# Kernel tuning notes

Measured on AMD Instinct MI355X. Metric: run time of the kernel, lower is better.

The kernel has to match this reference:

```python
import jax, jax.numpy as jnp
import numpy as np

TOKENS = 16384
HID = 2048


def _per_channel_scale(w, b):
    # scale per output channel, as in _apply_per_channel_scaling
    s = jnp.clip(jnp.max(jnp.abs(w), axis=1), 1e-6, None)  # [out]
    return w / s[:, None], b / s, s[None, :]  # scaled weight, scaled bias, scale row-vector


def setup_inputs() -> dict:
    key = jax.random.key(0)
    k = jax.random.split(key, 5)
    x = jax.random.normal(k[0], (TOKENS, HID), dtype=jnp.float32)
    w1_raw = jax.random.normal(k[1], (2 * HID, HID), dtype=jnp.float32) * 0.02
    b1_raw = jax.random.normal(k[2], (2 * HID,), dtype=jnp.float32) * 0.02
    w2_raw = jax.random.normal(k[3], (HID, 2 * HID), dtype=jnp.float32) * 0.02
    b2_raw = jax.random.normal(k[4], (HID,), dtype=jnp.float32) * 0.02
    w1, b1, s1 = _per_channel_scale(w1_raw, b1_raw)
    w2, b2, s2 = _per_channel_scale(w2_raw, b2_raw)
    return {"x": x, "w1": w1, "b1": b1, "s1": s1, "w2": w2, "b2": b2, "s2": s2}


def reference(x, w1, b1, s1, w2, b2, s2):
    # fc1 (scaled weights) -> per-channel dequant scale -> exact GELU -> fc2 -> scale
    h = (x @ w1.T + b1) * s1            # [T, 2H]
    h = jax.nn.gelu(h, approximate=False)
    y = (h @ w2.T + b2) * s2            # [T, H]
    return y
```

## Files before the change

### kernel.cpp

```cpp
#include <hip/hip_runtime.h>
#include <math.h>

typedef __attribute__((ext_vector_type(8))) short short8;
typedef __attribute__((ext_vector_type(4))) float f32x4;

#define GLOBAL_AS __attribute__((address_space(1)))
#define LDS_AS __attribute__((address_space(3)))

__device__ __forceinline__ unsigned short f2bf(float f) {
  union { float f; unsigned u; } v; v.f = f;
  unsigned r = v.u + 0x7fffu + ((v.u >> 16) & 1u);
  return (unsigned short)(r >> 16);
}

__global__ void cvt_f32_to_bf16(const float* __restrict__ in,
                                unsigned short* __restrict__ out, int n4) {
  int i = blockIdx.x * blockDim.x + threadIdx.x;
  if (i < n4) {
    const float4 v = ((const float4*)in)[i];
    ushort4 o;
    o.x = f2bf(v.x); o.y = f2bf(v.y); o.z = f2bf(v.z); o.w = f2bf(v.w);
    ((ushort4*)out)[i] = o;
  }
}

template <int EPI>
__global__ __launch_bounds__(512, 2) void gemm256_8ph(
    const unsigned short* __restrict__ A, const unsigned short* __restrict__ B,
    const float* __restrict__ bias, const float* __restrict__ scale,
    void* __restrict__ Cout, int M, int N, int K) {
  constexpr int BM = 256, BN = 256;
  __shared__ __attribute__((aligned(16))) unsigned short ldsA[4][8192];
  __shared__ __attribute__((aligned(16))) unsigned short ldsB[4][8192];

  const int NT = K >> 6;
  const int nTn = N / BN;
  const int bid = blockIdx.x;
  const int cpx = gridDim.x >> 3;
  const int wg = (bid & 7) * cpx + (bid >> 3);
  const int tm = wg / nTn, tn = wg % nTn;

  const int tid = threadIdx.x;
  const int w = tid >> 6, l = tid & 63;
  const int wr = w >> 2, wc = w & 3;
  const int lr = l & 15, g = l >> 4;

  const unsigned short* Ag = A + (size_t)tm * BM * K;
  const unsigned short* Bg = B + (size_t)tn * BN * K;

  size_t gs[2];
#pragma unroll
  for (int sgi = 0; sgi < 2; ++sgi) {
    int p = tid * 16 + sgi * 8192;
    int sp = p ^ (((p >> 7) & 7) << 4);
    gs[sgi] = (size_t)(sp >> 6) * K + ((sp & 63) >> 1);
  }
  const int ldsWaveOff = w * 512;

  auto STAGE = [&](int tau, int ks, const unsigned short* gb,
                   unsigned short (*slotArr)[8192]) {
    if (tau >= NT) return;
    unsigned short* sl = slotArr[(2 * tau + ks) & 3];
    const size_t ko = ((size_t)tau << 6) + (ks << 5);
    __builtin_amdgcn_global_load_lds((const GLOBAL_AS void*)(gb + gs[0] + ko),
                                     (LDS_AS void*)(sl + ldsWaveOff), 16, 0, 0);
    __builtin_amdgcn_global_load_lds((const GLOBAL_AS void*)(gb + gs[1] + ko),
                                     (LDS_AS void*)(sl + 4096 + ldsWaveOff), 16, 0, 0);
  };

  auto LD = [&](const unsigned short* slot, int row) -> short8 {
    int by = row * 64 + g * 16;
    by ^= ((by >> 7) & 7) << 4;
    return *(const short8*)((const char*)slot + by);
  };

  f32x4 acc[8][4] = {};

  STAGE(0, 0, Ag, ldsA); STAGE(0, 0, Bg, ldsB);
  STAGE(0, 1, Ag, ldsA); STAGE(0, 1, Bg, ldsB);
  STAGE(1, 0, Ag, ldsA); STAGE(1, 0, Bg, ldsB);
  asm volatile("s_waitcnt vmcnt(4)" ::: "memory");
  __builtin_amdgcn_s_barrier();

  for (int kt = 0; kt < NT; ++kt) {
    const unsigned short* As0 = ldsA[(2 * kt) & 3];
    const unsigned short* Bs0 = ldsB[(2 * kt) & 3];
    const unsigned short* As1 = ldsA[(2 * kt + 1) & 3];
    const unsigned short* Bs1 = ldsB[(2 * kt + 1) & 3];
    const int ar = wr * 128 + lr;
    const int br = wc * 64 + lr;
    short8 a[4], b[4];

#pragma unroll
    for (int m = 0; m < 4; ++m) a[m] = LD(As0, ar + m * 16);
#pragma unroll
    for (int n = 0; n < 4; ++n) b[n] = LD(Bs0, br + n * 16);
    STAGE(kt + 1, 1, Ag, ldsA);
    __builtin_amdgcn_s_barrier();
    __builtin_amdgcn_s_setprio(1);
#pragma unroll
    for (int m = 0; m < 4; ++m)
#pragma unroll
      for (int n = 0; n < 4; ++n)
        acc[m][n] = __builtin_amdgcn_mfma_f32_16x16x32_bf16(a[m], b[n], acc[m][n], 0, 0, 0);
    __builtin_amdgcn_s_setprio(0);
    __builtin_amdgcn_s_barrier();

#pragma unroll
    for (int m = 0; m < 4; ++m) a[m] = LD(As0, ar + 64 + m * 16);
    STAGE(kt + 1, 1, Bg, ldsB);
    __builtin_amdgcn_s_barrier();
    __builtin_amdgcn_s_setprio(1);
#pragma unroll
    for (int m = 0; m < 4; ++m)
#pragma unroll
      for (int n = 0; n < 4; ++n)
        acc[4 + m][n] = __builtin_amdgcn_mfma_f32_16x16x32_bf16(a[m], b[n], acc[4 + m][n], 0, 0, 0);
    __builtin_amdgcn_s_setprio(0);
    __builtin_amdgcn_s_barrier();

#pragma unroll
    for (int m = 0; m < 4; ++m) a[m] = LD(As1, ar + m * 16);
#pragma unroll
    for (int n = 0; n < 4; ++n) b[n] = LD(Bs1, br + n * 16);
    STAGE(kt + 2, 0, Ag, ldsA);
    __builtin_amdgcn_s_barrier();
    __builtin_amdgcn_s_setprio(1);
#pragma unroll
    for (int m = 0; m < 4; ++m)
#pragma unroll
      for (int n = 0; n < 4; ++n)
        acc[m][n] = __builtin_amdgcn_mfma_f32_16x16x32_bf16(a[m], b[n], acc[m][n], 0, 0, 0);
    __builtin_amdgcn_s_setprio(0);
    __builtin_amdgcn_s_barrier();

#pragma unroll
    for (int m = 0; m < 4; ++m) a[m] = LD(As1, ar + 64 + m * 16);
    STAGE(kt + 2, 0, Bg, ldsB);
    __builtin_amdgcn_s_barrier();
    __builtin_amdgcn_s_setprio(1);
#pragma unroll
    for (int m = 0; m < 4; ++m)
#pragma unroll
      for (int n = 0; n < 4; ++n)
        acc[4 + m][n] = __builtin_amdgcn_mfma_f32_16x16x32_bf16(a[m], b[n], acc[4 + m][n], 0, 0, 0);
    __builtin_amdgcn_s_setprio(0);
    if (kt + 2 < NT) { asm volatile("s_waitcnt vmcnt(4)" ::: "memory"); }
    else             { asm volatile("s_waitcnt vmcnt(0)" ::: "memory"); }
    __builtin_amdgcn_s_barrier();
  }

  const int orow = tm * BM + wr * 128;
  const int ocol = tn * BN + wc * 64;
  const int rsub = g * 4;
#pragma unroll
  for (int n = 0; n < 4; ++n) {
    const int gn = ocol + n * 16 + lr;
    const float bv = bias[gn];
    const float sv = scale[gn];
#pragma unroll
    for (int m = 0; m < 8; ++m) {
#pragma unroll
      for (int j = 0; j < 4; ++j) {
        const int gm = orow + m * 16 + rsub + j;
        float v = (acc[m][n][j] + bv) * sv;
        if (EPI == 0) {
          const float gl = 0.5f * v * (1.0f + erff(v * 0.70710678118654752440f));
          ((unsigned short*)Cout)[(size_t)gm * N + gn] = f2bf(gl);
        } else {
          ((float*)Cout)[(size_t)gm * N + gn] = v;
        }
      }
    }
  }
}

extern "C" void kernel_launch(void* const* d_in, const int* in_sizes, int n_in,
                              void* d_out, int out_size, void* d_ws, size_t ws_size,
                              hipStream_t stream) {
  const int T = 16384, H = 2048, H2 = 4096;
  const float* x  = (const float*)d_in[0];
  const float* w1 = (const float*)d_in[1];
  const float* b1 = (const float*)d_in[2];
  const float* s1 = (const float*)d_in[3];
  const float* w2 = (const float*)d_in[4];
  const float* b2 = (const float*)d_in[5];
  const float* s2 = (const float*)d_in[6];

  unsigned short* xb  = (unsigned short*)d_ws;
  unsigned short* w1b = xb  + (size_t)T  * H;
  unsigned short* w2b = w1b + (size_t)H2 * H;
  unsigned short* hb  = w2b + (size_t)H  * H2;

  int n4 = T * H / 4;
  cvt_f32_to_bf16<<<(n4 + 255) / 256, 256, 0, stream>>>(x, xb, n4);
  n4 = H2 * H / 4;
  cvt_f32_to_bf16<<<(n4 + 255) / 256, 256, 0, stream>>>(w1, w1b, n4);
  cvt_f32_to_bf16<<<(n4 + 255) / 256, 256, 0, stream>>>(w2, w2b, n4);

  gemm256_8ph<0><<<(T / 256) * (H2 / 256), 512, 0, stream>>>(
      xb, w1b, b1, s1, (void*)hb, T, H2, H);
  gemm256_8ph<1><<<(T / 256) * (H / 256), 512, 0, stream>>>(
      hb, w2b, b2, s2, d_out, T, H, H2);
}
```

Before: 870.0 us.

## Unroll GEMM main loop by two with constant LDS slot offsets

Unrolls the K loop two iterations at a time so all four LDS ring slots are compile-time constants. Global and LDS address bases are precomputed once, removing per-phase index and swizzle arithmetic. Each MFMA phase now waits on lgkmcnt(0) after its barrier, and the vmcnt waits are retuned for the new stage order, including a tail case. This adds code size and puts more weight on getting the pipeline waits right for odd K-tile counts.

```diff
diff --git a/kernel.cpp b/kernel.cpp
--- a/kernel.cpp
+++ b/kernel.cpp
@@ -30,8 +30,8 @@
     const float* __restrict__ bias, const float* __restrict__ scale,
     void* __restrict__ Cout, int M, int N, int K) {
   constexpr int BM = 256, BN = 256;
-  __shared__ __attribute__((aligned(16))) unsigned short ldsA[4][8192];
-  __shared__ __attribute__((aligned(16))) unsigned short ldsB[4][8192];
+  __shared__ __attribute__((aligned(16))) unsigned short ldsA[32768];
+  __shared__ __attribute__((aligned(16))) unsigned short ldsB[32768];
 
   const int NT = K >> 6;
   const int nTn = N / BN;
@@ -48,105 +48,119 @@
   const unsigned short* Ag = A + (size_t)tm * BM * K;
   const unsigned short* Bg = B + (size_t)tn * BN * K;
 
-  size_t gs[2];
-#pragma unroll
-  for (int sgi = 0; sgi < 2; ++sgi) {
-    int p = tid * 16 + sgi * 8192;
-    int sp = p ^ (((p >> 7) & 7) << 4);
-    gs[sgi] = (size_t)(sp >> 6) * K + ((sp & 63) >> 1);
-  }
+  size_t gs0, gs1;
+  {
+    int p0 = tid * 16, p1 = tid * 16 + 8192;
+    int sp0 = p0 ^ (((p0 >> 7) & 7) << 4);
+    int sp1 = p1 ^ (((p1 >> 7) & 7) << 4);
+    gs0 = (size_t)(sp0 >> 6) * K + ((sp0 & 63) >> 1);
+    gs1 = (size_t)(sp1 >> 6) * K + ((sp1 & 63) >> 1);
+  }
+  const unsigned short* pA0 = Ag + gs0; const unsigned short* pA1 = Ag + gs1;
+  const unsigned short* pB0 = Bg + gs0; const unsigned short* pB1 = Bg + gs1;
   const int ldsWaveOff = w * 512;
 
-  auto STAGE = [&](int tau, int ks, const unsigned short* gb,
-                   unsigned short (*slotArr)[8192]) {
-    if (tau >= NT) return;
-    unsigned short* sl = slotArr[(2 * tau + ks) & 3];
-    const size_t ko = ((size_t)tau << 6) + (ks << 5);
-    __builtin_amdgcn_global_load_lds((const GLOBAL_AS void*)(gb + gs[0] + ko),
-                                     (LDS_AS void*)(sl + ldsWaveOff), 16, 0, 0);
-    __builtin_amdgcn_global_load_lds((const GLOBAL_AS void*)(gb + gs[1] + ko),
-                                     (LDS_AS void*)(sl + 4096 + ldsWaveOff), 16, 0, 0);
-  };
-
-  auto LD = [&](const unsigned short* slot, int row) -> short8 {
-    int by = row * 64 + g * 16;
-    by ^= ((by >> 7) & 7) << 4;
-    return *(const short8*)((const char*)slot + by);
-  };
+#define STAGE_A(tau, ks, SLOT)                                                   \
+  if ((tau) < NT) {                                                              \
+    const size_t ko_ = ((size_t)(tau) << 6) + ((ks) << 5);                       \
+    __builtin_amdgcn_global_load_lds((const GLOBAL_AS void*)(pA0 + ko_),         \
+        (LDS_AS void*)(ldsA + (SLOT)*8192 + ldsWaveOff), 16, 0, 0);              \
+    __builtin_amdgcn_global_load_lds((const GLOBAL_AS void*)(pA1 + ko_),         \
+        (LDS_AS void*)(ldsA + (SLOT)*8192 + 4096 + ldsWaveOff), 16, 0, 0);       \
+  }
+#define STAGE_B(tau, ks, SLOT)                                                   \
+  if ((tau) < NT) {                                                              \
+    const size_t ko_ = ((size_t)(tau) << 6) + ((ks) << 5);                       \
+    __builtin_amdgcn_global_load_lds((const GLOBAL_AS void*)(pB0 + ko_),         \
+        (LDS_AS void*)(ldsB + (SLOT)*8192 + ldsWaveOff), 16, 0, 0);              \
+    __builtin_amdgcn_global_load_lds((const GLOBAL_AS void*)(pB1 + ko_),         \
+        (LDS_AS void*)(ldsB + (SLOT)*8192 + 4096 + ldsWaveOff), 16, 0, 0);       \
+  }
+
+  int ab = ((wr * 128 + lr) << 6) + (g << 4);
+  int aoff = ab ^ (((ab >> 7) & 7) << 4);
+  int bb = ((wc * 64 + lr) << 6) + (g << 4);
+  int boff = bb ^ (((bb >> 7) & 7) << 4);
+  const char* ldsAb = (const char*)ldsA + aoff;
+  const char* ldsBb = (const char*)ldsB + boff;
+#define LDA8(S, H, m) (*(const short8*)(ldsAb + (S)*16384 + (H)*4096 + (m)*1024))
+#define LDB8(S, n)    (*(const short8*)(ldsBb + (S)*16384 + (n)*1024))
 
   f32x4 acc[8][4] = {};
-
-  STAGE(0, 0, Ag, ldsA); STAGE(0, 0, Bg, ldsB);
-  STAGE(0, 1, Ag, ldsA); STAGE(0, 1, Bg, ldsB);
-  STAGE(1, 0, Ag, ldsA); STAGE(1, 0, Bg, ldsB);
+  short8 a[4], b[4];
+
+#define OPEN_MFMA(ROW0)                                                          \
+  __builtin_amdgcn_s_barrier();                                                  \
+  asm volatile("s_waitcnt lgkmcnt(0)" ::: "memory");                             \
+  __builtin_amdgcn_s_setprio(1);                                                 \
+  _Pragma("unroll") for (int m = 0; m < 4; ++m)                                  \
+  _Pragma("unroll") for (int n = 0; n < 4; ++n)                                  \
+    acc[(ROW0) + m][n] = __builtin_amdgcn_mfma_f32_16x16x32_bf16(                \
+        a[m], b[n], acc[(ROW0) + m][n], 0, 0, 0);                                \
+  __builtin_amdgcn_s_setprio(0);
+
+  STAGE_A(0, 0, 0) STAGE_B(0, 0, 0)
+  STAGE_A(0, 1, 1) STAGE_B(0, 1, 1)
+  STAGE_A(1, 0, 2) STAGE_B(1, 0, 2)
   asm volatile("s_waitcnt vmcnt(4)" ::: "memory");
   __builtin_amdgcn_s_barrier();
 
-  for (int kt = 0; kt < NT; ++kt) {
-    const unsigned short* As0 = ldsA[(2 * kt) & 3];
-    const unsigned short* Bs0 = ldsB[(2 * kt) & 3];
-    const unsigned short* As1 = ldsA[(2 * kt + 1) & 3];
-    const unsigned short* Bs1 = ldsB[(2 * kt + 1) & 3];
-    const int ar = wr * 128 + lr;
-    const int br = wc * 64 + lr;
-    short8 a[4], b[4];
-
-#pragma unroll
-    for (int m = 0; m < 4; ++m) a[m] = LD(As0, ar + m * 16);
-#pragma unroll
-    for (int n = 0; n < 4; ++n) b[n] = LD(Bs0, br + n * 16);
-    STAGE(kt + 1, 1, Ag, ldsA);
-    __builtin_amdgcn_s_barrier();
-    __builtin_amdgcn_s_setprio(1);
-#pragma unroll
-    for (int m = 0; m < 4; ++m)
-#pragma unroll
-      for (int n = 0; n < 4; ++n)
-        acc[m][n] = __builtin_amdgcn_mfma_f32_16x16x32_bf16(a[m], b[n], acc[m][n], 0, 0, 0);
-    __builtin_amdgcn_s_setprio(0);
-    __builtin_amdgcn_s_barrier();
-
-#pragma unroll
-    for (int m = 0; m < 4; ++m) a[m] = LD(As0, ar + 64 + m * 16);
-    STAGE(kt + 1, 1, Bg, ldsB);
-    __builtin_amdgcn_s_barrier();
-    __builtin_amdgcn_s_setprio(1);
-#pragma unroll
-    for (int m = 0; m < 4; ++m)
-#pragma unroll
-      for (int n = 0; n < 4; ++n)
-        acc[4 + m][n] = __builtin_amdgcn_mfma_f32_16x16x32_bf16(a[m], b[n], acc[4 + m][n], 0, 0, 0);
-    __builtin_amdgcn_s_setprio(0);
-    __builtin_amdgcn_s_barrier();
-
-#pragma unroll
-    for (int m = 0; m < 4; ++m) a[m] = LD(As1, ar + m * 16);
-#pragma unroll
-    for (int n = 0; n < 4; ++n) b[n] = LD(Bs1, br + n * 16);
-    STAGE(kt + 2, 0, Ag, ldsA);
-    __builtin_amdgcn_s_barrier();
-    __builtin_amdgcn_s_setprio(1);
-#pragma unroll
-    for (int m = 0; m < 4; ++m)
-#pragma unroll
-      for (int n = 0; n < 4; ++n)
-        acc[m][n] = __builtin_amdgcn_mfma_f32_16x16x32_bf16(a[m], b[n], acc[m][n], 0, 0, 0);
-    __builtin_amdgcn_s_setprio(0);
-    __builtin_amdgcn_s_barrier();
-
-#pragma unroll
-    for (int m = 0; m < 4; ++m) a[m] = LD(As1, ar + 64 + m * 16);
-    STAGE(kt + 2, 0, Bg, ldsB);
-    __builtin_amdgcn_s_barrier();
-    __builtin_amdgcn_s_setprio(1);
-#pragma unroll
-    for (int m = 0; m < 4; ++m)
-#pragma unroll
-      for (int n = 0; n < 4; ++n)
-        acc[4 + m][n] = __builtin_amdgcn_mfma_f32_16x16x32_bf16(a[m], b[n], acc[4 + m][n], 0, 0, 0);
-    __builtin_amdgcn_s_setprio(0);
-    if (kt + 2 < NT) { asm volatile("s_waitcnt vmcnt(4)" ::: "memory"); }
-    else             { asm volatile("s_waitcnt vmcnt(0)" ::: "memory"); }
+  for (int kt = 0; kt < NT; kt += 2) {
+    const bool full = (kt + 2 < NT);
+#pragma unroll
+    for (int m = 0; m < 4; ++m) a[m] = LDA8(0, 0, m);
+#pragma unroll
+    for (int n = 0; n < 4; ++n) b[n] = LDB8(0, n);
+    STAGE_A(kt + 1, 1, 3)
+    OPEN_MFMA(0)
+    __builtin_amdgcn_s_barrier();
+#pragma unroll
+    for (int m = 0; m < 4; ++m) a[m] = LDA8(0, 1, m);
+    STAGE_B(kt + 1, 1, 3)
+    OPEN_MFMA(4)
+    asm volatile("s_waitcnt vmcnt(4)" ::: "memory");
+    __builtin_amdgcn_s_barrier();
+#pragma unroll
+    for (int m = 0; m < 4; ++m) a[m] = LDA8(1, 0, m);
+#pragma unroll
+    for (int n = 0; n < 4; ++n) b[n] = LDB8(1, n);
+    STAGE_A(kt + 2, 0, 0)
+    OPEN_MFMA(0)
+    __builtin_amdgcn_s_barrier();
+#pragma unroll
+    for (int m = 0; m < 4; ++m) a[m] = LDA8(1, 1, m);
+    STAGE_B(kt + 2, 0, 0)
+    OPEN_MFMA(4)
+    if (full) { asm volatile("s_waitcnt vmcnt(4)" ::: "memory"); }
+    else      { asm volatile("s_waitcnt vmcnt(2)" ::: "memory"); }
+    __builtin_amdgcn_s_barrier();
+#pragma unroll
+    for (int m = 0; m < 4; ++m) a[m] = LDA8(2, 0, m);
+#pragma unroll
+    for (int n = 0; n < 4; ++n) b[n] = LDB8(2, n);
+    STAGE_A(kt + 2, 1, 1)
+    OPEN_MFMA(0)
+    __builtin_amdgcn_s_barrier();
+#pragma unroll
+    for (int m = 0; m < 4; ++m) a[m] = LDA8(2, 1, m);
+    STAGE_B(kt + 2, 1, 1)
+    OPEN_MFMA(4)
+    if (full) { asm volatile("s_waitcnt vmcnt(4)" ::: "memory"); }
+    else      { asm volatile("s_waitcnt vmcnt(0)" ::: "memory"); }
+    __builtin_amdgcn_s_barrier();
+#pragma unroll
+    for (int m = 0; m < 4; ++m) a[m] = LDA8(3, 0, m);
+#pragma unroll
+    for (int n = 0; n < 4; ++n) b[n] = LDB8(3, n);
+    STAGE_A(kt + 3, 0, 2)
+    OPEN_MFMA(0)
+    __builtin_amdgcn_s_barrier();
+#pragma unroll
+    for (int m = 0; m < 4; ++m) a[m] = LDA8(3, 1, m);
+    STAGE_B(kt + 3, 0, 2)
+    OPEN_MFMA(4)
+    if (full) { asm volatile("s_waitcnt vmcnt(4)" ::: "memory"); }
+    else      { asm volatile("s_waitcnt vmcnt(0)" ::: "memory"); }
     __builtin_amdgcn_s_barrier();
   }
 
@@ -173,6 +187,11 @@
       }
     }
   }
+#undef STAGE_A
+#undef STAGE_B
+#undef LDA8
+#undef LDB8
+#undef OPEN_MFMA
 }
 
 extern "C" void kernel_launch(void* const* d_in, const int* in_sizes, int n_in,
```

Result: faster. 851.9 us (-2.1%).
